# Kernel tuning notes

Measured on AMD Instinct MI355X. Metric: run time of the kernel, lower is better.

## Reference

```python
import jax, jax.numpy as jnp
import numpy as np

B, D, DK = 16384, 1024, 1024


def setup_inputs() -> dict:
    key = jax.random.key(0)
    ks = jax.random.split(key, 11)
    return {
        "x": jax.random.normal(ks[0], (B, D), jnp.float32),
        "x_prev": jax.random.normal(ks[1], (B, D), jnp.float32),
        "num": jax.random.uniform(ks[2], (B, DK), jnp.float32),
        "den": jax.random.uniform(ks[3], (B, DK), jnp.float32) + 1.0,
        "Wk": jax.random.normal(ks[4], (DK, D), jnp.float32) * (D ** -0.5),
        "bk": jnp.zeros((DK,), jnp.float32),
        "mix_k": jax.random.uniform(ks[5], (), jnp.float32),
        "Wf": jax.random.normal(ks[6], (D, DK), jnp.float32) * (DK ** -0.5),
        "bf": jnp.zeros((D,), jnp.float32),
        "bonus": jax.random.normal(ks[7], (DK,), jnp.float32) * 0.1,
        "decay": jnp.float32(0.2),
    }


def reference(x, x_prev, num, den, Wk, bk, mix_k, Wf, bf, bonus, decay):
    # MixingLinear: Linear(mix*x + (1-mix)*x_prev). Source uses Kmaker for
    # K, R and V, so all three equal this single projection (faithful to code).
    mixed = mix_k * x + (1.0 - mix_k) * x_prev          # [B, D]
    K = mixed @ Wk.T + bk                                # [B, DK]; K == R == V
    e_bk = jnp.exp(bonus + K)                            # [B, DK]
    wkv = (num + e_bk * K) / (den + e_bk)                # V = K
    rwkv = jax.nn.sigmoid(K) * wkv                       # R = K
    w = jnp.exp(-jnp.exp(decay))                         # scalar time-decay
    eK = jnp.exp(K)
    num_new = w * num + eK * K                           # V = K
    den_new = w * den + eK
    out = rwkv @ Wf.T + bf                               # [B, D]
    return out, num_new, den_new
```

## Files before the change

### kernel.cpp

```cpp
#include <hip/hip_runtime.h>
#include <cstdint>

#define DEV static __device__ __forceinline__
#define WAITVM(N) asm volatile("s_waitcnt vmcnt(" #N ")" ::: "memory")

typedef float f32x4 __attribute__((ext_vector_type(4)));
typedef short bf16x8 __attribute__((ext_vector_type(8)));

constexpr int Bsz = 16384;
constexpr int Dd  = 1024;
constexpr int DKd = 1024;

DEV unsigned short f2bf(float f) {
    uint32_t u = __builtin_bit_cast(uint32_t, f);
    u += 0x7FFFu + ((u >> 16) & 1u);
    return (unsigned short)(u >> 16);
}

DEV void async_lds16(const void* g, void* l) {
    __builtin_amdgcn_global_load_lds(
        (const __attribute__((address_space(1))) void*)g,
        (__attribute__((address_space(3))) void*)l,
        16, 0, 0);
}

__global__ void k_prep(const float4* __restrict__ x, const float4* __restrict__ xp,
                       const float* __restrict__ mixp,
                       const float4* __restrict__ Wk, const float4* __restrict__ Wf,
                       unsigned short* __restrict__ mixed,
                       unsigned short* __restrict__ WkB,
                       unsigned short* __restrict__ WfB) {
    constexpr int n_mix = Bsz * Dd / 4;
    constexpr int n_w   = DKd * Dd / 4;
    constexpr int total = n_mix + 2 * n_w;
    const float m = *mixp, m1 = 1.0f - m;
    int i = blockIdx.x * blockDim.x + threadIdx.x;
    const int st = gridDim.x * blockDim.x;
    for (; i < total; i += st) {
        float4 a;
        unsigned short* dst;
        int idx;
        if (i < n_mix) {
            float4 xa = x[i], xb = xp[i];
            a.x = m * xa.x + m1 * xb.x;
            a.y = m * xa.y + m1 * xb.y;
            a.z = m * xa.z + m1 * xb.z;
            a.w = m * xa.w + m1 * xb.w;
            dst = mixed; idx = i;
        } else if (i < n_mix + n_w) {
            a = Wk[i - n_mix]; dst = WkB; idx = i - n_mix;
        } else {
            a = Wf[i - n_mix - n_w]; dst = WfB; idx = i - n_mix - n_w;
        }
        ushort4 o;
        o.x = f2bf(a.x); o.y = f2bf(a.y); o.z = f2bf(a.z); o.w = f2bf(a.w);
        reinterpret_cast<ushort4*>(dst)[idx] = o;
    }
}

template <int EPI>
__global__ __launch_bounds__(512, 2)
void k_gemm(const unsigned short* __restrict__ A,
            const unsigned short* __restrict__ Bw,
            const float* __restrict__ bias,
            const float* __restrict__ num, const float* __restrict__ den,
            const float* __restrict__ bonus, const float* __restrict__ decayp,
            float* __restrict__ o0, float* __restrict__ o1,
            unsigned short* __restrict__ orw)
{
    __shared__ __align__(16) unsigned short As[2][2][256 * 32];
    __shared__ __align__(16) unsigned short Bs[2][2][256 * 32];

    const int tid = threadIdx.x;
    const int bid = (int)blockIdx.x;
    const int wg  = (bid & 7) * 32 + (bid >> 3);
    const int cb  = wg & 3;
    const int rb  = wg >> 2;
    const int row0 = rb * 256;
    const int col0 = cb * 256;

    const int lane = tid & 63;
    const int wid  = tid >> 6;
    const int wr = wid >> 2, wc = wid & 3;
    const int l16 = lane & 15, lq = lane >> 4;

    const int r0   = tid >> 2;
    const int glog = (tid & 3) ^ (r0 & 3) ^ ((r0 >> 2) & 3);
    const unsigned short* pa0 = A  + (size_t)(row0 + r0) * 1024 + glog * 8;
    const unsigned short* pa1 = A  + (size_t)(row0 + r0 + 128) * 1024 + glog * 8;
    const unsigned short* pb0 = Bw + (size_t)(col0 + r0) * 1024 + glog * 8;
    const unsigned short* pb1 = Bw + (size_t)(col0 + r0 + 128) * 1024 + glog * 8;

    const int pg    = lq ^ (l16 & 3) ^ ((l16 >> 2) & 3);
    const int abase = (wr * 128 + l16) * 32 + pg * 8;
    const int bbase = (wc * 64 + l16) * 32 + pg * 8;

    f32x4 acc[8][4] = {};

    auto stage = [&](int buf, int kk, int t) {
        const int off = t * 64 + kk * 32;
        async_lds16(pa0 + off, &As[buf][kk][tid * 8]);
        async_lds16(pa1 + off, &As[buf][kk][(tid + 512) * 8]);
        async_lds16(pb0 + off, &Bs[buf][kk][tid * 8]);
        async_lds16(pb1 + off, &Bs[buf][kk][(tid + 512) * 8]);
    };

    auto compute = [&](int buf, int kk) {
        const unsigned short* Ar = &As[buf][kk][abase];
        const unsigned short* Br = &Bs[buf][kk][bbase];
        bf16x8 af[8], bfr[4];
#pragma unroll
        for (int n = 0; n < 4; ++n)
            bfr[n] = *reinterpret_cast<const bf16x8*>(Br + n * 512);
#pragma unroll
        for (int m = 0; m < 8; ++m)
            af[m] = *reinterpret_cast<const bf16x8*>(Ar + m * 512);
        __builtin_amdgcn_s_setprio(1);
#pragma unroll
        for (int m = 0; m < 8; ++m)
#pragma unroll
            for (int n = 0; n < 4; ++n)
                acc[m][n] = __builtin_amdgcn_mfma_f32_16x16x32_bf16(
                    af[m], bfr[n], acc[m][n], 0, 0, 0);
        __builtin_amdgcn_s_setprio(0);
    };

    stage(0, 0, 0); stage(0, 1, 0); stage(1, 0, 1); stage(1, 1, 1);
    WAITVM(12);
    __builtin_amdgcn_s_barrier();
    __builtin_amdgcn_sched_barrier(0);

#pragma unroll 1
    for (int t = 0; t < 14; ++t) {
        const int buf = t & 1;
        compute(buf, 0);
        WAITVM(8);
        __builtin_amdgcn_s_barrier();
        __builtin_amdgcn_sched_barrier(0);
        stage(buf, 0, t + 2);
        compute(buf, 1);
        WAITVM(8);
        __builtin_amdgcn_s_barrier();
        __builtin_amdgcn_sched_barrier(0);
        stage(buf, 1, t + 2);
    }
    compute(0, 0);
    WAITVM(8);  __builtin_amdgcn_s_barrier(); __builtin_amdgcn_sched_barrier(0);
    compute(0, 1);
    WAITVM(4);  __builtin_amdgcn_s_barrier(); __builtin_amdgcn_sched_barrier(0);
    compute(1, 0);
    WAITVM(0);  __builtin_amdgcn_s_barrier(); __builtin_amdgcn_sched_barrier(0);
    compute(1, 1);

    const int baserow = row0 + wr * 128 + lq * 4;
    const int basecol = col0 + wc * 64 + l16;

    if constexpr (EPI == 1) {
        const float w_decay = __expf(-__expf(*decayp));
        float cbias[4], cebon[4];
#pragma unroll
        for (int n = 0; n < 4; ++n) {
            cbias[n] = bias[basecol + n * 16];
            cebon[n] = __expf(bonus[basecol + n * 16]);
        }
#pragma unroll
        for (int m = 0; m < 8; ++m) {
#pragma unroll
            for (int r = 0; r < 4; ++r) {
                const size_t rowoff = (size_t)(baserow + m * 16 + r) * 1024;
#pragma unroll
                for (int n = 0; n < 4; ++n) {
                    const size_t idx = rowoff + basecol + n * 16;
                    const float Kv  = acc[m][n][r] + cbias[n];
                    const float eK  = __expf(Kv);
                    const float ebk = cebon[n] * eK;
                    const float nb  = num[idx];
                    const float db  = den[idx];
                    const float wkv = (nb + ebk * Kv) * __builtin_amdgcn_rcpf(db + ebk);
                    const float sig = eK * __builtin_amdgcn_rcpf(1.0f + eK);
                    o0[idx]  = w_decay * nb + eK * Kv;
                    o1[idx]  = w_decay * db + eK;
                    orw[idx] = f2bf(sig * wkv);
                }
            }
        }
    } else {
        float cbias[4];
#pragma unroll
        for (int n = 0; n < 4; ++n) cbias[n] = bias[basecol + n * 16];
#pragma unroll
        for (int m = 0; m < 8; ++m) {
#pragma unroll
            for (int r = 0; r < 4; ++r) {
                const size_t rowoff = (size_t)(baserow + m * 16 + r) * 1024;
#pragma unroll
                for (int n = 0; n < 4; ++n)
                    o0[rowoff + basecol + n * 16] = acc[m][n][r] + cbias[n];
            }
        }
    }
}

extern "C" void kernel_launch(void* const* d_in, const int* in_sizes, int n_in,
                              void* d_out, int out_size, void* d_ws, size_t ws_size,
                              hipStream_t stream) {
    const float* x     = (const float*)d_in[0];
    const float* xprev = (const float*)d_in[1];
    const float* num   = (const float*)d_in[2];
    const float* den   = (const float*)d_in[3];
    const float* Wk    = (const float*)d_in[4];
    const float* bk    = (const float*)d_in[5];
    const float* mixk  = (const float*)d_in[6];
    const float* Wf    = (const float*)d_in[7];
    const float* bf_   = (const float*)d_in[8];
    const float* bonus = (const float*)d_in[9];
    const float* decay = (const float*)d_in[10];

    float* out    = (float*)d_out;
    float* numnew = out + (size_t)Bsz * Dd;
    float* dennew = numnew + (size_t)Bsz * DKd;

    char* ws = (char*)d_ws;
    unsigned short* mixed = (unsigned short*)ws;
    unsigned short* WkB   = (unsigned short*)(ws + (size_t)Bsz * Dd * 2);
    unsigned short* WfB   = WkB + (size_t)DKd * Dd;
    unsigned short* rwkv  = WfB + (size_t)Dd * DKd;

    k_prep<<<2048, 256, 0, stream>>>((const float4*)x, (const float4*)xprev, mixk,
                                     (const float4*)Wk, (const float4*)Wf,
                                     mixed, WkB, WfB);

    const int grid = (Bsz / 256) * (DKd / 256);
    k_gemm<1><<<grid, 512, 0, stream>>>(mixed, WkB, bk, num, den, bonus, decay,
                                        numnew, dennew, rwkv);
    k_gemm<0><<<grid, 512, 0, stream>>>(rwkv, WfB, bf_, nullptr, nullptr, nullptr,
                                        nullptr, out, nullptr, nullptr);
}
```

Measured before the change: 184.6 us.

## Restructure GEMM K-loop into 4-slot ring buffer with 3-deep prefetch

```diff
diff --git a/kernel.cpp b/kernel.cpp
--- a/kernel.cpp
+++ b/kernel.cpp
@@ -59,7 +59,7 @@
 }
 
 template <int EPI>
-__global__ __launch_bounds__(512, 2)
+__global__ __launch_bounds__(512)
 void k_gemm(const unsigned short* __restrict__ A,
             const unsigned short* __restrict__ Bw,
             const float* __restrict__ bias,
@@ -68,8 +68,8 @@
             float* __restrict__ o0, float* __restrict__ o1,
             unsigned short* __restrict__ orw)
 {
-    __shared__ __align__(16) unsigned short As[2][2][256 * 32];
-    __shared__ __align__(16) unsigned short Bs[2][2][256 * 32];
+    __shared__ __align__(16) unsigned short As[4][256 * 32];
+    __shared__ __align__(16) unsigned short Bs[4][256 * 32];
 
     const int tid = threadIdx.x;
     const int bid = (int)blockIdx.x;
@@ -97,24 +97,32 @@
 
     f32x4 acc[8][4] = {};
 
-    auto stage = [&](int buf, int kk, int t) {
-        const int off = t * 64 + kk * 32;
-        async_lds16(pa0 + off, &As[buf][kk][tid * 8]);
-        async_lds16(pa1 + off, &As[buf][kk][(tid + 512) * 8]);
-        async_lds16(pb0 + off, &Bs[buf][kk][tid * 8]);
-        async_lds16(pb1 + off, &Bs[buf][kk][(tid + 512) * 8]);
+    auto stage = [&](int t) {
+        const int slot = t & 3;
+        const int off  = t * 32;
+        async_lds16(pa0 + off, &As[slot][tid * 8]);
+        async_lds16(pa1 + off, &As[slot][(tid + 512) * 8]);
+        async_lds16(pb0 + off, &Bs[slot][tid * 8]);
+        async_lds16(pb1 + off, &Bs[slot][(tid + 512) * 8]);
     };
 
-    auto compute = [&](int buf, int kk) {
-        const unsigned short* Ar = &As[buf][kk][abase];
-        const unsigned short* Br = &Bs[buf][kk][bbase];
+    stage(0); stage(1); stage(2);
+    WAITVM(8);
+    __builtin_amdgcn_s_barrier();
+    __builtin_amdgcn_sched_barrier(0);
+
+#pragma unroll 1
+    for (int t = 0; t < 32; ++t) {
+        if (t < 29) stage(t + 3);
+        const unsigned short* Ab = &As[t & 3][abase];
+        const unsigned short* Bb = &Bs[t & 3][bbase];
         bf16x8 af[8], bfr[4];
 #pragma unroll
         for (int n = 0; n < 4; ++n)
-            bfr[n] = *reinterpret_cast<const bf16x8*>(Br + n * 512);
+            bfr[n] = *reinterpret_cast<const bf16x8*>(Bb + n * 512);
 #pragma unroll
         for (int m = 0; m < 8; ++m)
-            af[m] = *reinterpret_cast<const bf16x8*>(Ar + m * 512);
+            af[m] = *reinterpret_cast<const bf16x8*>(Ab + m * 512);
         __builtin_amdgcn_s_setprio(1);
 #pragma unroll
         for (int m = 0; m < 8; ++m)
@@ -123,34 +131,14 @@
                 acc[m][n] = __builtin_amdgcn_mfma_f32_16x16x32_bf16(
                     af[m], bfr[n], acc[m][n], 0, 0, 0);
         __builtin_amdgcn_s_setprio(0);
-    };
-
-    stage(0, 0, 0); stage(0, 1, 0); stage(1, 0, 1); stage(1, 1, 1);
-    WAITVM(12);
-    __builtin_amdgcn_s_barrier();
-    __builtin_amdgcn_sched_barrier(0);
-
-#pragma unroll 1
-    for (int t = 0; t < 14; ++t) {
-        const int buf = t & 1;
-        compute(buf, 0);
-        WAITVM(8);
-        __builtin_amdgcn_s_barrier();
-        __builtin_amdgcn_sched_barrier(0);
-        stage(buf, 0, t + 2);
-        compute(buf, 1);
-        WAITVM(8);
-        __builtin_amdgcn_s_barrier();
-        __builtin_amdgcn_sched_barrier(0);
-        stage(buf, 1, t + 2);
+        if (t < 29)      { WAITVM(8); }
+        else if (t == 29){ WAITVM(4); }
+        else if (t == 30){ WAITVM(0); }
+        if (t < 31) {
+            __builtin_amdgcn_s_barrier();
+            __builtin_amdgcn_sched_barrier(0);
+        }
     }
-    compute(0, 0);
-    WAITVM(8);  __builtin_amdgcn_s_barrier(); __builtin_amdgcn_sched_barrier(0);
-    compute(0, 1);
-    WAITVM(4);  __builtin_amdgcn_s_barrier(); __builtin_amdgcn_sched_barrier(0);
-    compute(1, 0);
-    WAITVM(0);  __builtin_amdgcn_s_barrier(); __builtin_amdgcn_sched_barrier(0);
-    compute(1, 1);
 
     const int baserow = row0 + wr * 128 + lq * 4;
     const int basecol = col0 + wc * 64 + l16;
```

Measured after the change: 205.2 us. 1.11x slower.

## Use 4-slot single-barrier LDS pipeline with setprio for first GEMM

Applied to the files above, without the earlier changes.

```diff
diff --git a/kernel.cpp b/kernel.cpp
--- a/kernel.cpp
+++ b/kernel.cpp
@@ -58,15 +58,125 @@
     }
 }
 
-template <int EPI>
+__global__ __launch_bounds__(512)
+void k_gemm1(const unsigned short* __restrict__ A,
+             const unsigned short* __restrict__ Bw,
+             const float* __restrict__ bias,
+             const float* __restrict__ num, const float* __restrict__ den,
+             const float* __restrict__ bonus, const float* __restrict__ decayp,
+             float* __restrict__ o0, float* __restrict__ o1,
+             unsigned short* __restrict__ orw)
+{
+    __shared__ __align__(16) unsigned short As[4][256 * 32];
+    __shared__ __align__(16) unsigned short Bs[4][256 * 32];
+
+    const int tid = threadIdx.x;
+    const int bid = (int)blockIdx.x;
+    const int wg  = (bid & 7) * 32 + (bid >> 3);
+    const int cb  = wg & 3;
+    const int rb  = wg >> 2;
+    const int row0 = rb * 256;
+    const int col0 = cb * 256;
+
+    const int lane = tid & 63;
+    const int wid  = tid >> 6;
+    const int wr = wid >> 2, wc = wid & 3;
+    const int l16 = lane & 15, lq = lane >> 4;
+
+    const int r0   = tid >> 2;
+    const int glog = (tid & 3) ^ (r0 & 3) ^ ((r0 >> 2) & 3);
+    const unsigned short* pa0 = A  + (size_t)(row0 + r0) * 1024 + glog * 8;
+    const unsigned short* pa1 = A  + (size_t)(row0 + r0 + 128) * 1024 + glog * 8;
+    const unsigned short* pb0 = Bw + (size_t)(col0 + r0) * 1024 + glog * 8;
+    const unsigned short* pb1 = Bw + (size_t)(col0 + r0 + 128) * 1024 + glog * 8;
+
+    const int pg    = lq ^ (l16 & 3) ^ ((l16 >> 2) & 3);
+    const int abase = (wr * 128 + l16) * 32 + pg * 8;
+    const int bbase = (wc * 64 + l16) * 32 + pg * 8;
+
+    f32x4 acc[8][4] = {};
+
+    auto stage = [&](int t) {
+        const int slot = t & 3;
+        const int off  = t * 32;
+        async_lds16(pa0 + off, &As[slot][tid * 8]);
+        async_lds16(pa1 + off, &As[slot][(tid + 512) * 8]);
+        async_lds16(pb0 + off, &Bs[slot][tid * 8]);
+        async_lds16(pb1 + off, &Bs[slot][(tid + 512) * 8]);
+    };
+
+    stage(0); stage(1); stage(2);
+    WAITVM(8);
+    __builtin_amdgcn_s_barrier();
+    __builtin_amdgcn_sched_barrier(0);
+
+#pragma unroll 1
+    for (int t = 0; t < 32; ++t) {
+        if (t < 29) stage(t + 3);
+        const unsigned short* Ab = &As[t & 3][abase];
+        const unsigned short* Bb = &Bs[t & 3][bbase];
+        bf16x8 af[8], bfr[4];
+#pragma unroll
+        for (int n = 0; n < 4; ++n)
+            bfr[n] = *reinterpret_cast<const bf16x8*>(Bb + n * 512);
+#pragma unroll
+        for (int m = 0; m < 8; ++m)
+            af[m] = *reinterpret_cast<const bf16x8*>(Ab + m * 512);
+        __builtin_amdgcn_s_setprio(1);
+#pragma unroll
+        for (int m = 0; m < 8; ++m)
+#pragma unroll
+            for (int n = 0; n < 4; ++n)
+                acc[m][n] = __builtin_amdgcn_mfma_f32_16x16x32_bf16(
+                    af[m], bfr[n], acc[m][n], 0, 0, 0);
+        __builtin_amdgcn_s_setprio(0);
+        if (t < 29)      { WAITVM(8); }
+        else if (t == 29){ WAITVM(4); }
+        else if (t == 30){ WAITVM(0); }
+        if (t < 31) {
+            __builtin_amdgcn_s_barrier();
+            __builtin_amdgcn_sched_barrier(0);
+        }
+    }
+
+    const int baserow = row0 + wr * 128 + lq * 4;
+    const int basecol = col0 + wc * 64 + l16;
+
+    const float w_decay = __expf(-__expf(*decayp));
+    float cbias[4], cebon[4];
+#pragma unroll
+    for (int n = 0; n < 4; ++n) {
+        cbias[n] = bias[basecol + n * 16];
+        cebon[n] = __expf(bonus[basecol + n * 16]);
+    }
+#pragma unroll
+    for (int m = 0; m < 8; ++m) {
+#pragma unroll
+        for (int r = 0; r < 4; ++r) {
+            const size_t rowoff = (size_t)(baserow + m * 16 + r) * 1024;
+#pragma unroll
+            for (int n = 0; n < 4; ++n) {
+                const size_t idx = rowoff + basecol + n * 16;
+                const float Kv  = acc[m][n][r] + cbias[n];
+                const float eK  = __expf(Kv);
+                const float ebk = cebon[n] * eK;
+                const float nb  = num[idx];
+                const float db  = den[idx];
+                const float wkv = (nb + ebk * Kv) * __builtin_amdgcn_rcpf(db + ebk);
+                const float sig = eK * __builtin_amdgcn_rcpf(1.0f + eK);
+                o0[idx]  = w_decay * nb + eK * Kv;
+                o1[idx]  = w_decay * db + eK;
+                orw[idx] = f2bf(sig * wkv);
+            }
+        }
+    }
+}
+
 __global__ __launch_bounds__(512, 2)
-void k_gemm(const unsigned short* __restrict__ A,
-            const unsigned short* __restrict__ Bw,
-            const float* __restrict__ bias,
-            const float* __restrict__ num, const float* __restrict__ den,
-            const float* __restrict__ bonus, const float* __restrict__ decayp,
-            float* __restrict__ o0, float* __restrict__ o1,
-            unsigned short* __restrict__ orw)
+void k_gemm2(const unsigned short* __restrict__ A,
+             const unsigned short* __restrict__ Bw,
+             const float* __restrict__ bias,
+             float* __restrict__ o0)
 {
     __shared__ __align__(16) unsigned short As[2][2][256 * 32];
     __shared__ __align__(16) unsigned short Bs[2][2][256 * 32];
@@ -155,48 +265,17 @@
     const int baserow = row0 + wr * 128 + lq * 4;
     const int basecol = col0 + wc * 64 + l16;
 
-    if constexpr (EPI == 1) {
-        const float w_decay = __expf(-__expf(*decayp));
-        float cbias[4], cebon[4];
-#pragma unroll
-        for (int n = 0; n < 4; ++n) {
-            cbias[n] = bias[basecol + n * 16];
-            cebon[n] = __expf(bonus[basecol + n * 16]);
-        }
-#pragma unroll
-        for (int m = 0; m < 8; ++m) {
-#pragma unroll
-            for (int r = 0; r < 4; ++r) {
-                const size_t rowoff = (size_t)(baserow + m * 16 + r) * 1024;
-#pragma unroll
-                for (int n = 0; n < 4; ++n) {
-                    const size_t idx = rowoff + basecol + n * 16;
-                    const float Kv  = acc[m][n][r] + cbias[n];
-                    const float eK  = __expf(Kv);
-                    const float ebk = cebon[n] * eK;
-                    const float nb  = num[idx];
-                    const float db  = den[idx];
-                    const float wkv = (nb + ebk * Kv) * __builtin_amdgcn_rcpf(db + ebk);
-                    const float sig = eK * __builtin_amdgcn_rcpf(1.0f + eK);
-                    o0[idx]  = w_decay * nb + eK * Kv;
-                    o1[idx]  = w_decay * db + eK;
-                    orw[idx] = f2bf(sig * wkv);
-                }
-            }
-        }
-    } else {
-        float cbias[4];
-#pragma unroll
-        for (int n = 0; n < 4; ++n) cbias[n] = bias[basecol + n * 16];
-#pragma unroll
-        for (int m = 0; m < 8; ++m) {
-#pragma unroll
-            for (int r = 0; r < 4; ++r) {
-                const size_t rowoff = (size_t)(baserow + m * 16 + r) * 1024;
-#pragma unroll
-                for (int n = 0; n < 4; ++n)
-                    o0[rowoff + basecol + n * 16] = acc[m][n][r] + cbias[n];
-            }
+    float cbias[4];
+#pragma unroll
+    for (int n = 0; n < 4; ++n) cbias[n] = bias[basecol + n * 16];
+#pragma unroll
+    for (int m = 0; m < 8; ++m) {
+#pragma unroll
+        for (int r = 0; r < 4; ++r) {
+            const size_t rowoff = (size_t)(baserow + m * 16 + r) * 1024;
+#pragma unroll
+            for (int n = 0; n < 4; ++n)
+                o0[rowoff + basecol + n * 16] = acc[m][n][r] + cbias[n];
         }
     }
 }
@@ -231,8 +310,7 @@
                                      mixed, WkB, WfB);
 
     const int grid = (Bsz / 256) * (DKd / 256);
-    k_gemm<1><<<grid, 512, 0, stream>>>(mixed, WkB, bk, num, den, bonus, decay,
-                                        numnew, dennew, rwkv);
-    k_gemm<0><<<grid, 512, 0, stream>>>(rwkv, WfB, bf_, nullptr, nullptr, nullptr,
-                                        nullptr, out, nullptr, nullptr);
-}
+    k_gemm1<<<grid, 512, 0, stream>>>(mixed, WkB, bk, num, den, bonus, decay,
+                                      numnew, dennew, rwkv);
+    k_gemm2<<<grid, 512, 0, stream>>>(rwkv, WfB, bf_, out);
+}
```

Result: slower. 192.4 us (+4.2%).
